# Optimization experiments

Measured on AMD Instinct MI355X. Metric: run time of the kernel, lower is better.

The kernel has to match this reference:

```python
import jax, jax.numpy as jnp
import numpy as np
import math

B, N, D = 4, 4096, 256


def setup_inputs() -> dict:
    key = jax.random.key(0)
    k0, k1, k2, k3 = jax.random.split(key, 4)
    # kaiming-uniform-like init for the square weight matrices
    bound = math.sqrt(6.0 / D)
    return {
        "x": jax.random.normal(k0, (B, N, D), dtype=jnp.float32),
        "Wq": jax.random.uniform(k1, (D, D), dtype=jnp.float32, minval=-bound, maxval=bound),
        "Wk": jax.random.uniform(k2, (D, D), dtype=jnp.float32, minval=-bound, maxval=bound),
        "Wv": jax.random.uniform(k3, (D, D), dtype=jnp.float32, minval=-bound, maxval=bound),
    }


def reference(x, Wq, Wk, Wv):
    # x: [B, N, D]; W*: [D, D]
    q = x @ Wq.T
    k = x @ Wk.T
    v = x @ Wv.T
    n = x.shape[1]
    d_k = x.shape[2]
    # mask = triu(ones, diagonal=1): 1 strictly above the diagonal.
    # (1 - mask) is 1 on and below the diagonal, so those positions get -1e10
    # (faithful to the original: it masks the diagonal and past, keeps future).
    mask = jnp.triu(jnp.ones((n, n), dtype=x.dtype), k=1)
    scale = jnp.asarray(1.0 / math.sqrt(d_k), dtype=x.dtype)
    s = (jnp.einsum('bnd,bmd->bnm', q, k) - (1.0 - mask) * 1e10) * scale
    # Faithful quirk: softmax over dim=1 (the query/row axis), not the last axis.
    s = jax.nn.softmax(s, axis=1)
    return jnp.einsum('bnm,bmd->bnd', s, v)
```

## Files before the change

### kernel.cpp

```cpp
#include <hip/hip_runtime.h>
#include <hip/hip_bf16.h>


typedef float f32x4 __attribute__((ext_vector_type(4)));
typedef __bf16 bf16x8 __attribute__((ext_vector_type(8)));
typedef __bf16 bf16x4 __attribute__((ext_vector_type(4)));

#define MFMA16(a, b, c) __builtin_amdgcn_mfma_f32_16x16x32_bf16((a), (b), (c), 0, 0, 0)

constexpr int SEQ = 4096;
constexpr int DIM = 256;

__host__ __device__ inline int tri(int x) { return (x * (x + 1)) >> 1; }

__device__ __forceinline__ void gl16(const __bf16* g, __bf16* l) {
  __builtin_amdgcn_global_load_lds((const __attribute__((address_space(1))) void*)g,
                                   (__attribute__((address_space(3))) void*)l, 16, 0, 0);
}

__global__ void k_prep(const float* __restrict__ Wq, const float* __restrict__ Wk,
                       const float* __restrict__ Wv, __bf16* __restrict__ Wb,
                       float* __restrict__ colsum) {
  int i = blockIdx.x * 256 + threadIdx.x;
  if (i < 3 * 65536) {
    const float* src = (i < 65536) ? Wq : (i < 131072 ? Wk : Wv);
    Wb[i] = (__bf16)src[i & 65535];
  }
  if (i < 4 * SEQ) colsum[i] = 0.f;
}

__global__ __launch_bounds__(256, 2) void k_qkv(const float* __restrict__ x,
                                                const __bf16* __restrict__ Wb,
                                                __bf16* __restrict__ Qb,
                                                __bf16* __restrict__ Kb,
                                                __bf16* __restrict__ Vb) {
  __shared__ __bf16 wsh[64][264];
  const int t = threadIdx.x, lane = t & 63, w = t >> 6;
  const int ln = lane & 15, quad = lane >> 4, q8 = quad * 8;
  const int i0 = blockIdx.x * 64;
  bf16x8 xa[8];
#pragma unroll
  for (int kf = 0; kf < 8; ++kf) {
    const float* src = &x[(size_t)(i0 + w * 16 + ln) * DIM + kf * 32 + q8];
    float4 v0 = *(const float4*)&src[0];
    float4 v1 = *(const float4*)&src[4];
    xa[kf] = bf16x8{(__bf16)v0.x, (__bf16)v0.y, (__bf16)v0.z, (__bf16)v0.w,
                    (__bf16)v1.x, (__bf16)v1.y, (__bf16)v1.z, (__bf16)v1.w};
  }
  for (int zj = 0; zj < 12; ++zj) {
    const int z = zj >> 2, j0 = (zj & 3) * 64;
    const __bf16* W = Wb + z * 65536 + j0 * 256;
    bf16x8 stg[8];
#pragma unroll
    for (int i = 0; i < 8; ++i) stg[i] = *(const bf16x8*)&W[(t + i * 256) * 8];
    __syncthreads();
#pragma unroll
    for (int i = 0; i < 8; ++i)
      *(bf16x8*)&wsh[(t >> 5) + i * 8][(t & 31) * 8] = stg[i];
    __syncthreads();
    f32x4 acc[4] = {};
#pragma unroll
    for (int kf = 0; kf < 8; ++kf) {
      bf16x8 bb[4];
#pragma unroll
      for (int tj = 0; tj < 4; ++tj)
        bb[tj] = *(bf16x8*)&wsh[tj * 16 + ln][kf * 32 + q8];
#pragma unroll
      for (int tj = 0; tj < 4; ++tj) acc[tj] = MFMA16(xa[kf], bb[tj], acc[tj]);
    }
    __bf16* Out = (z == 0) ? Qb : (z == 1 ? Kb : Vb);
#pragma unroll
    for (int tj = 0; tj < 4; ++tj)
#pragma unroll
      for (int r = 0; r < 4; ++r) {
        int row = i0 + w * 16 + quad * 4 + r;
        int col = j0 + tj * 16 + ln;
        Out[(size_t)row * DIM + col] = (__bf16)acc[tj][r];
      }
  }
}

__global__ __launch_bounds__(256, 2) void k_scores(const __bf16* __restrict__ Qb,
                                                   const __bf16* __restrict__ Kb,
                                                   __bf16* __restrict__ E,
                                                   float* __restrict__ colsum,
                                                   int mtLo, int triLo, int ntiles) {
  __shared__ __bf16 qsh[2 * 64 * 256];
  const int t = threadIdx.x, lane = t & 63, w = t >> 6;
  const int ln = lane & 15, quad = lane >> 4, q8 = quad * 8;
  const int bid = blockIdx.x;
  const int b = (bid & 7) >> 1;
  const int rest = ((bid >> 3) << 1) | (bid & 1);
  const int mt = mtLo + (rest >> 2);
  const int s = rest & 3;
  if (s > mt) return;
  const int m0 = mt * 64;
  const __bf16* Qp = Qb + (size_t)b * SEQ * DIM;
  const __bf16* Kp = Kb + (size_t)b * SEQ * DIM;
  bf16x8 kb[8];
#pragma unroll
  for (int kf = 0; kf < 8; ++kf)
    kb[kf] = *(const bf16x8*)&Kp[(size_t)(m0 + w * 16 + ln) * DIM + kf * 32 + q8];
  auto stageq = [&](int ncv, int buf) {
    const __bf16* src = Qp + (size_t)ncv * 16384;
#pragma unroll
    for (int i2 = 0; i2 < 8; ++i2) {
      int sl = t + i2 * 256;
      int row = sl >> 5, g = sl & 31;
      gl16(&src[row * 256 + ((g ^ (row & 15)) << 3)], &qsh[buf * 16384 + sl * 8]);
    }
  };
  float csum4[4] = {0.f, 0.f, 0.f, 0.f};
  const int P16 = w * 2 + (quad >> 1);
  const int sub = (quad & 1) * 4;
  int nc = s, cur = 0;
  if (nc <= mt) stageq(nc, 0);
  for (; nc <= mt; nc += 4, cur ^= 1) {
    __syncthreads();
    if (nc + 4 <= mt) stageq(nc + 4, cur ^ 1);
    f32x4 accST[4] = {};
#pragma unroll
    for (int kf = 0; kf < 8; ++kf) {
#pragma unroll
      for (int tn = 0; tn < 4; ++tn) {
        int row = tn * 16 + ln;
        bf16x8 bq = *(const bf16x8*)&qsh[cur * 16384 + row * 256 +
                                         (((kf * 4 + quad) ^ ln) << 3)];
        accST[tn] = MFMA16(kb[kf], bq, accST[tn]);
      }
    }
    __bf16* Et = E + ((size_t)b * ntiles + (tri(mt) - triLo) + nc) * 4096;
#pragma unroll
    for (int tn = 0; tn < 4; ++tn) {
      int nl = tn * 16 + ln;
      int n_g = nc * 64 + nl;
      int mb = m0 + w * 16 + quad * 4;
      bf16x4 pk;
#pragma unroll
      for (int r = 0; r < 4; ++r) {
        float e = (n_g < mb + r) ? __expf(accST[tn][r] * 0.0625f) : 0.f;
        csum4[r] += e;
        pk[r] = (__bf16)e;
      }
      *(bf16x4*)&Et[nl * 64 + ((P16 ^ (nl & 7)) << 3) + sub] = pk;
    }
  }
#pragma unroll
  for (int r = 0; r < 4; ++r) {
    float v = csum4[r];
    v += __shfl_xor(v, 1);
    v += __shfl_xor(v, 2);
    v += __shfl_xor(v, 4);
    v += __shfl_xor(v, 8);
    if (ln == 0) atomicAdd(&colsum[b * SEQ + m0 + w * 16 + quad * 4 + r], v);
  }
}

__global__ void k_vpt(const __bf16* __restrict__ Vb, const float* __restrict__ colsum,
                      __bf16* __restrict__ VpT, int mtLo) {
  __shared__ __bf16 tile[64][72];
  const int t = threadIdx.x;
  const int b = blockIdx.z;
  const int mblk = mtLo + blockIdx.x;
  const int m0 = mblk * 64, d0 = blockIdx.y * 64;
  {
    int row = t >> 2, part = t & 3;
    float cs = colsum[b * SEQ + m0 + row];
    float inv = (m0 + row == 0) ? (1.0f / 4096.0f) : (1.0f / cs);
#pragma unroll
    for (int i = 0; i < 2; ++i) {
      int c = part * 2 + i;
      bf16x8 v = *(const bf16x8*)&Vb[(size_t)(b * SEQ + m0 + row) * DIM + d0 + c * 8];
      bf16x8 o;
#pragma unroll
      for (int j = 0; j < 8; ++j) o[j] = (__bf16)((float)v[j] * inv);
      *(bf16x8*)&tile[row][c * 8] = o;
    }
  }
  __syncthreads();
  {
    int row = t >> 2, part = t & 3;
#pragma unroll
    for (int i = 0; i < 2; ++i) {
      int c = part * 2 + i;
      bf16x8 o;
#pragma unroll
      for (int j = 0; j < 8; ++j) o[j] = tile[c * 8 + j][row];
      *(bf16x8*)&VpT[(size_t)((b * 64 + mblk) * 256 + d0 + row) * 64 +
                     ((c ^ (row & 7)) << 3)] = o;
    }
  }
}

__global__ __launch_bounds__(256, 4) void k_pv(const __bf16* __restrict__ E,
                                               const __bf16* __restrict__ VpT,
                                               const __bf16* __restrict__ Vb,
                                               float* __restrict__ out,
                                               int mtLo, int mtHi, int triLo,
                                               int ntiles) {
  __shared__ __bf16 esh[2 * 32 * 64];
  __shared__ __bf16 vsh[2 * 128 * 64];
  const int t = threadIdx.x, lane = t & 63, w = t >> 6;
  const int ln = lane & 15, quad = lane >> 4;
  const int bid = blockIdx.x;
  const int b = (bid & 7) >> 1;
  const int idx = ((bid >> 3) << 1) | (bid & 1);
  const int p = idx >> 1, dh = idx & 1;
  const int nt32 = (p & 1) ? (2 * mtHi - 1 - (p >> 1)) : (p >> 1);
  const int nc = nt32 >> 1, half = nt32 & 1;
  const int mtStart = (nc > mtLo) ? nc : mtLo;
  const int n0 = nt32 * 32;
  const __bf16* Vt = VpT + (size_t)b * SEQ * DIM;
  auto stageE = [&](int msv, int buf) {
    const __bf16* ep =
        E + ((size_t)b * ntiles + (tri(msv) - triLo) + nc) * 4096 + half * 2048;
    gl16(&ep[t * 8], &esh[buf * 2048 + t * 8]);
  };
  auto stageVp = [&](int msv, int buf) {
    const __bf16* vp = Vt + (size_t)msv * 16384 + dh * 8192;
#pragma unroll
    for (int i2 = 0; i2 < 4; ++i2) {
      int sl = t + i2 * 256;
      gl16(&vp[sl * 8], &vsh[buf * 8192 + sl * 8]);
    }
  };
  f32x4 accO[2][2] = {};
  int cur = 0;
  stageE(mtHi - 1, 0);
  stageVp(mtHi - 1, 0);
  for (int ms = mtHi - 1; ms >= mtStart; --ms, cur ^= 1) {
    __syncthreads();
    if (ms - 1 >= mtStart) { stageE(ms - 1, cur ^ 1); stageVp(ms - 1, cur ^ 1); }
#pragma unroll
    for (int kf = 0; kf < 2; ++kf) {
      bf16x8 aa[2], bb[2];
#pragma unroll
      for (int tn = 0; tn < 2; ++tn) {
        int row = tn * 16 + ln;
        aa[tn] = *(const bf16x8*)&esh[cur * 2048 + row * 64 +
                                      (((kf * 4 + quad) ^ (row & 7)) << 3)];
      }
#pragma unroll
      for (int td = 0; td < 2; ++td) {
        int rl = w * 32 + td * 16 + ln;
        bb[td] = *(const bf16x8*)&vsh[cur * 8192 + rl * 64 +
                                      (((kf * 4 + quad) ^ (rl & 7)) << 3)];
      }
#pragma unroll
      for (int tn = 0; tn < 2; ++tn)
#pragma unroll
        for (int td = 0; td < 2; ++td)
          accO[tn][td] = MFMA16(aa[tn], bb[td], accO[tn][td]);
    }
  }
  float* Op = out + ((size_t)b << 20);
  const __bf16* V0 = Vb + ((size_t)b << 20);
  const bool init = (nc >= mtLo);
#pragma unroll
  for (int tn = 0; tn < 2; ++tn)
#pragma unroll
    for (int td = 0; td < 2; ++td) {
      int col = dh * 128 + w * 32 + td * 16 + ln;
      float c0 = init ? (float)V0[col] * (1.0f / 4096.0f) : 0.f;
#pragma unroll
      for (int r = 0; r < 4; ++r) {
        int row = n0 + tn * 16 + quad * 4 + r;
        float* pp = &Op[(size_t)row * DIM + col];
        float v = accO[tn][td][r] + c0;
        if (!init) v += *pp;
        *pp = v;
      }
    }
}

extern "C" void kernel_launch(void* const* d_in, const int* in_sizes, int n_in,
                              void* d_out, int out_size, void* d_ws, size_t ws_size,
                              hipStream_t stream) {
  const float* x = (const float*)d_in[0];
  const float* Wq = (const float*)d_in[1];
  const float* Wk = (const float*)d_in[2];
  const float* Wv = (const float*)d_in[3];
  float* out = (float*)d_out;
  char* ws = (char*)d_ws;
  __bf16* Qb = (__bf16*)(ws);
  __bf16* Kb = (__bf16*)(ws + (8u << 20));
  __bf16* Vb = (__bf16*)(ws + (16u << 20));
  __bf16* VpT = (__bf16*)(ws + (24u << 20));
  float* colsum = (float*)(ws + (32u << 20));
  __bf16* Wb = (__bf16*)(ws + (32u << 20) + (1u << 16));
  const size_t base2 = (32u << 20) + (1u << 16) + (384u << 10);
  __bf16* E = (__bf16*)(ws + base2);
  const size_t fullE = (size_t)4 * 2080 * 4096 * sizeof(__bf16);
  int nPass, lo[3], hi[3];
  if (ws_size >= base2 + fullE) {
    nPass = 1; lo[0] = 0; hi[0] = 64;
  } else {
    nPass = 3;
    lo[0] = 0;  hi[0] = 37;
    lo[1] = 37; hi[1] = 53;
    lo[2] = 53; hi[2] = 64;
  }

  k_prep<<<dim3(768), dim3(256), 0, stream>>>(Wq, Wk, Wv, Wb, colsum);
  k_qkv<<<dim3(256), dim3(256), 0, stream>>>(x, Wb, Qb, Kb, Vb);
  for (int p = 0; p < nPass; ++p) {
    const int nmt = hi[p] - lo[p];
    const int triLo = tri(lo[p]);
    const int ntiles = tri(hi[p]) - triLo;
    k_scores<<<dim3(16 * nmt), dim3(256), 0, stream>>>(Qb, Kb, E, colsum,
                                                       lo[p], triLo, ntiles);
    k_vpt<<<dim3(nmt, 4, 4), dim3(256), 0, stream>>>(Vb, colsum, VpT, lo[p]);
    k_pv<<<dim3(16 * hi[p]), dim3(256), 0, stream>>>(E, VpT, Vb, out,
                                                     lo[p], hi[p], triLo, ntiles);
  }
}
```

Measured before the change: 179.8 us.

## Store E in MFMA fragment order and load directly to registers in PV

The score kernel now writes exp tiles of E in a per-lane MFMA fragment layout instead of a swizzled row-major layout. The PV kernel can then load its A operands straight from global memory into registers with coalesced 16-byte loads, double-buffered in registers, rather than staging them through LDS. This cuts LDS traffic and shared memory use and may raise occupancy. In exchange, all four waves redundantly load the same E fragments from global/L2, and the prefetch depends on register latency hiding.

```diff
diff --git a/kernel.cpp b/kernel.cpp
--- a/kernel.cpp
+++ b/kernel.cpp
@@ -111,8 +111,9 @@
     }
   };
   float csum4[4] = {0.f, 0.f, 0.f, 0.f};
-  const int P16 = w * 2 + (quad >> 1);
-  const int sub = (quad & 1) * 4;
+  const int fragBase = (w >> 1) * 4;
+  const int lane_c = ln + 16 * ((w & 1) * 2 + (quad >> 1));
+  const int j0 = (quad & 1) * 4;
   int nc = s, cur = 0;
   if (nc <= mt) stageq(nc, 0);
   for (; nc <= mt; nc += 4, cur ^= 1) {
@@ -132,8 +133,7 @@
     __bf16* Et = E + ((size_t)b * ntiles + (tri(mt) - triLo) + nc) * 4096;
 #pragma unroll
     for (int tn = 0; tn < 4; ++tn) {
-      int nl = tn * 16 + ln;
-      int n_g = nc * 64 + nl;
+      int n_g = nc * 64 + tn * 16 + ln;
       int mb = m0 + w * 16 + quad * 4;
       bf16x4 pk;
 #pragma unroll
@@ -142,7 +142,7 @@
         csum4[r] += e;
         pk[r] = (__bf16)e;
       }
-      *(bf16x4*)&Et[nl * 64 + ((P16 ^ (nl & 7)) << 3) + sub] = pk;
+      *(bf16x4*)&Et[((fragBase + tn) * 64 + lane_c) * 8 + j0] = pk;
     }
   }
 #pragma unroll
@@ -198,7 +198,6 @@
                                                float* __restrict__ out,
                                                int mtLo, int mtHi, int triLo,
                                                int ntiles) {
-  __shared__ __bf16 esh[2 * 32 * 64];
   __shared__ __bf16 vsh[2 * 128 * 64];
   const int t = threadIdx.x, lane = t & 63, w = t >> 6;
   const int ln = lane & 15, quad = lane >> 4;
@@ -211,10 +210,14 @@
   const int mtStart = (nc > mtLo) ? nc : mtLo;
   const int n0 = nt32 * 32;
   const __bf16* Vt = VpT + (size_t)b * SEQ * DIM;
-  auto stageE = [&](int msv, int buf) {
-    const __bf16* ep =
-        E + ((size_t)b * ntiles + (tri(msv) - triLo) + nc) * 4096 + half * 2048;
-    gl16(&ep[t * 8], &esh[buf * 2048 + t * 8]);
+  const __bf16* Ebase = E + ((size_t)b * ntiles - triLo + nc) * 4096;
+  auto loadE = [&](int msv, bf16x8 e[2][2]) {
+    const __bf16* ep = Ebase + (size_t)tri(msv) * 4096;
+#pragma unroll
+    for (int kf = 0; kf < 2; ++kf)
+#pragma unroll
+      for (int tn = 0; tn < 2; ++tn)
+        e[tn][kf] = *(const bf16x8*)&ep[((kf * 4 + half * 2 + tn) * 64 + lane) * 8];
   };
   auto stageVp = [&](int msv, int buf) {
     const __bf16* vp = Vt + (size_t)msv * 16384 + dh * 8192;
@@ -225,21 +228,19 @@
     }
   };
   f32x4 accO[2][2] = {};
+  bf16x8 eN[2][2], eC[2][2];
   int cur = 0;
-  stageE(mtHi - 1, 0);
-  stageVp(mtHi - 1, 0);
+  if (mtHi - 1 >= mtStart) { loadE(mtHi - 1, eN); stageVp(mtHi - 1, 0); }
   for (int ms = mtHi - 1; ms >= mtStart; --ms, cur ^= 1) {
     __syncthreads();
-    if (ms - 1 >= mtStart) { stageE(ms - 1, cur ^ 1); stageVp(ms - 1, cur ^ 1); }
+#pragma unroll
+    for (int tn = 0; tn < 2; ++tn)
+#pragma unroll
+      for (int kf = 0; kf < 2; ++kf) eC[tn][kf] = eN[tn][kf];
+    if (ms - 1 >= mtStart) { loadE(ms - 1, eN); stageVp(ms - 1, cur ^ 1); }
 #pragma unroll
     for (int kf = 0; kf < 2; ++kf) {
-      bf16x8 aa[2], bb[2];
-#pragma unroll
-      for (int tn = 0; tn < 2; ++tn) {
-        int row = tn * 16 + ln;
-        aa[tn] = *(const bf16x8*)&esh[cur * 2048 + row * 64 +
-                                      (((kf * 4 + quad) ^ (row & 7)) << 3)];
-      }
+      bf16x8 bb[2];
 #pragma unroll
       for (int td = 0; td < 2; ++td) {
         int rl = w * 32 + td * 16 + ln;
@@ -250,7 +251,7 @@
       for (int tn = 0; tn < 2; ++tn)
 #pragma unroll
         for (int td = 0; td < 2; ++td)
-          accO[tn][td] = MFMA16(aa[tn], bb[td], accO[tn][td]);
+          accO[tn][td] = MFMA16(eC[tn][kf], bb[td], accO[tn][td]);
     }
   }
   float* Op = out + ((size_t)b << 20);
```

New measurement: 191.0 us. 1.06x slower.
